# Optimization experiments

Hardware: AMD Instinct MI355X
Metric: run time of the kernel (lower is better)

The kernel has to match this reference:

```python
import jax, jax.numpy as jnp
import numpy as np

B, S, E, D, H = 4, 1024, 1024, 1024, 16   # batch, dec_seq, enc_seq, d_model, n_heads
DH = D // H
DFF = 4096
EPS = 1e-5


def setup_inputs() -> dict:
    key = jax.random.key(0)
    ks = jax.random.split(key, 16)
    w = lambda k, shp: (jax.random.normal(k, shp, dtype=jnp.float32) * 0.02)
    return {
        "x": jax.random.normal(ks[0], (B, S, D), dtype=jnp.float32),
        "enc_x": jax.random.normal(ks[1], (B, E, D), dtype=jnp.float32),
        # masked self-attn (fused qkv)
        "w_qkv": w(ks[2], (D, 3 * D)), "b_qkv": jnp.zeros((3 * D,), jnp.float32),
        "w_sa_o": w(ks[3], (D, D)), "b_sa_o": jnp.zeros((D,), jnp.float32),
        # cross-attn
        "w_q": w(ks[4], (D, D)), "b_q": jnp.zeros((D,), jnp.float32),
        "w_k": w(ks[5], (D, D)), "b_k": jnp.zeros((D,), jnp.float32),
        "w_v": w(ks[6], (D, D)), "b_v": jnp.zeros((D,), jnp.float32),
        "w_ca_o": w(ks[7], (D, D)), "b_ca_o": jnp.zeros((D,), jnp.float32),
        # ffn
        "w1": w(ks[8], (D, DFF)), "b1": jnp.zeros((DFF,), jnp.float32),
        "w2": w(ks[9], (DFF, D)), "b2": jnp.zeros((D,), jnp.float32),
        # layernorms
        "g1": jnp.ones((D,), jnp.float32), "be1": jnp.zeros((D,), jnp.float32),
        "g2": jnp.ones((D,), jnp.float32), "be2": jnp.zeros((D,), jnp.float32),
        "g3": jnp.ones((D,), jnp.float32), "be3": jnp.zeros((D,), jnp.float32),
    }


def _layernorm(x, g, b):
    mean = jnp.mean(x, axis=-1, keepdims=True)
    var = jnp.mean(jnp.square(x - mean), axis=-1, keepdims=True)  # unbiased=False
    return g * (x - mean) / jnp.sqrt(var + EPS) + b


def _masked_self_attn(x, w_qkv, b_qkv, w_o, b_o):
    b, s, d = x.shape
    qkv = x @ w_qkv + b_qkv                            # [b,s,3D]
    # Faithful to torch: view as [b,s,H,3*DH] then chunk last dim (interleaved per-head).
    qkv = qkv.reshape(b, s, H, 3 * DH).transpose(0, 2, 1, 3)   # [b,H,s,3DH]
    q, k, v = jnp.split(qkv, 3, axis=-1)               # each [b,H,s,DH]
    scores = jnp.einsum('bhqd,bhkd->bhqk', q, k) / jnp.sqrt(jnp.float32(DH))
    mask = jnp.triu(jnp.ones((s, s), dtype=bool), k=1)
    scores = jnp.where(mask, -jnp.inf, scores)
    attn = jax.nn.softmax(scores, axis=-1)
    out = jnp.einsum('bhqk,bhkd->bhqd', attn, v)       # [b,H,s,DH]
    out = out.transpose(0, 2, 1, 3).reshape(b, s, d)
    return out @ w_o + b_o


def _cross_attn(dec_x, enc_x, w_q, b_q, w_k, b_k, w_v, b_v, w_o, b_o):
    b, sq, d = dec_x.shape
    sk = enc_x.shape[1]
    q = (dec_x @ w_q + b_q).reshape(b, sq, H, DH).transpose(0, 2, 1, 3)
    k = (enc_x @ w_k + b_k).reshape(b, sk, H, DH).transpose(0, 2, 1, 3)
    v = (enc_x @ w_v + b_v).reshape(b, sk, H, DH).transpose(0, 2, 1, 3)
    scores = jnp.einsum('bhqd,bhkd->bhqk', q, k) / jnp.sqrt(jnp.float32(DH))
    attn = jax.nn.softmax(scores, axis=-1)
    out = jnp.einsum('bhqk,bhkd->bhqd', attn, v).transpose(0, 2, 1, 3).reshape(b, sq, d)
    return out @ w_o + b_o


def reference(x, enc_x, w_qkv, b_qkv, w_sa_o, b_sa_o,
              w_q, b_q, w_k, b_k, w_v, b_v, w_ca_o, b_ca_o,
              w1, b1, w2, b2, g1, be1, g2, be2, g3, be3):
    h = _layernorm(x + _masked_self_attn(x, w_qkv, b_qkv, w_sa_o, b_sa_o), g1, be1)
    h = _layernorm(h + _cross_attn(h, enc_x, w_q, b_q, w_k, b_k, w_v, b_v, w_ca_o, b_ca_o), g2, be2)
    ffn = jax.nn.gelu(h @ w1 + b1, approximate=False) @ w2 + b2  # torch F.gelu default = exact
    return _layernorm(h + ffn, g3, be3)
```

## Files before the change

### kernel.cpp

```cpp
#include <hip/hip_runtime.h>

#define BB 4
#define SS 1024
#define DD 1024
#define HH 16
#define DHH 64
#define DFF 4096
#define MROWS 4096
#define NEG_BIG (-1e30f)
#define LOG2E 1.4426950408889634f
#define SCL_L2E 0.1803368801111244f

typedef float  f32x4  __attribute__((ext_vector_type(4)));
typedef __bf16 bf16x8 __attribute__((ext_vector_type(8)));
typedef __bf16 bf16x4 __attribute__((ext_vector_type(4)));

#define DEV __device__ __forceinline__

DEV void glds16(const __bf16* g, __bf16* l) {
  __builtin_amdgcn_global_load_lds((__attribute__((address_space(1))) void*)(g),
                                   (__attribute__((address_space(3))) void*)(l),
                                   16, 0, 0);
}

DEV float sanit(float v) {
  return fminf(fmaxf(v, -1e30f), 1e30f);
}

DEV float gelu_f(float v) {
  const float z  = fabsf(v) * 0.70710678118654752f;
  const float t  = __builtin_amdgcn_rcpf(1.f + 0.3275911f * z);
  float poly = ((((1.061405429f * t - 1.453152027f) * t + 1.421413741f) * t
                 - 0.284496736f) * t + 0.254829592f) * t;
  float er = 1.f - poly * __expf(-z * z);
  er = copysignf(er, v);
  return 0.5f * v * (1.f + er);
}

__global__ __launch_bounds__(256) void cvt_bf16(const float* __restrict__ src,
                                                __bf16* __restrict__ dst)
{
  const int idx = blockIdx.x * 256 + threadIdx.x;
  const f32x4 v = ((const f32x4*)src)[idx];
  bf16x4 o;
#pragma unroll
  for (int i = 0; i < 4; i++) o[i] = (__bf16)v[i];
  ((bf16x4*)dst)[idx] = o;
}

__global__ __launch_bounds__(256) void wtrans(const float* __restrict__ src,
                                              __bf16* __restrict__ dst,
                                              int K, int N)
{
  __shared__ float t[64][65];
  const int k0 = blockIdx.y * 64, n0 = blockIdx.x * 64;
  const int c = threadIdx.x & 63, r0 = threadIdx.x >> 6;
#pragma unroll
  for (int i = 0; i < 16; i++) {
    const int r = r0 * 16 + i;
    t[r][c] = src[(size_t)(k0 + r) * N + n0 + c];
  }
  __syncthreads();
#pragma unroll
  for (int i = 0; i < 16; i++) {
    const int r = r0 * 16 + i;
    dst[(size_t)(n0 + r) * K + k0 + c] = (__bf16)t[c][r];
  }
}

__global__ __launch_bounds__(256) void vtrans(const __bf16* __restrict__ src,
                                              int stride, int colMul, int colAdd,
                                              __bf16* __restrict__ dst)
{
  __shared__ __bf16 t[64][66];
  const int bh = blockIdx.y, b = bh >> 4, h = bh & 15;
  const int s0 = blockIdx.x * 64;
  const int c = threadIdx.x & 63, r0 = threadIdx.x >> 6;
  const __bf16* sp = src + (size_t)(b * SS) * stride + h * colMul + colAdd;
#pragma unroll
  for (int i = 0; i < 16; i++) {
    const int s = r0 * 16 + i;
    t[s][c] = sp[(size_t)(s0 + s) * stride + c];
  }
  __syncthreads();
  __bf16* dp = dst + (size_t)bh * 64 * 1024;
#pragma unroll
  for (int i = 0; i < 16; i++) {
    const int d = r0 * 16 + i;
    dp[(size_t)d * 1024 + s0 + c] = t[c][d];
  }
}

template<int MODE, int SPLIT>
__global__ __launch_bounds__(512) void gemm256(
    const __bf16* __restrict__ A, const __bf16* __restrict__ Bt,
    const float* __restrict__ bias, void* __restrict__ Cout,
    int N, int K)
{
  __shared__ __align__(16) __bf16 As[2][2][2][128 * 32];
  __shared__ __align__(16) __bf16 Bs[2][2][2][128 * 32];

  const int gx = gridDim.x;
  const int nwg = gx * gridDim.y;
  int idl = blockIdx.x + gx * blockIdx.y;
  idl = (idl & 7) * (nwg >> 3) + (idl >> 3);
  const int bn = (idl % gx) * 256, bm = (idl / gx) * 256;
  const int kz = SPLIT ? blockIdx.z : 0;
  const int Keff = SPLIT ? (K >> 1) : K;
  const int kOff = SPLIT ? kz * Keff : 0;

  const int tid = threadIdx.x, wid = tid >> 6, lane = tid & 63;
  const int quad = lane >> 4, ln = lane & 15;
  const int wr = (wid >> 2) * 128, wc = (wid & 3) * 64;
  const int mh = wid >> 2;
  const int nh = (wid & 3) >> 1;
  const int rbB = wc & 64;
  const int sw = ln >> 2;

  const int srow = tid >> 2;
  const int scol = ((tid & 3) ^ ((tid >> 4) & 3)) * 8;
  const __bf16* gA = A  + (size_t)(bm + srow) * K + kOff + scol;
  const __bf16* gB = Bt + (size_t)(bn + srow) * K + kOff + scol;
  const int dOff = tid * 8;

#define STG(bf_, MATG, MATS, kh_, kt_) do {                                         \
    glds16(MATG + (size_t)(kt_) * 64 + (kh_) * 32,                 &MATS[bf_][0][kh_][0] + dOff); \
    glds16(MATG + (size_t)128 * K + (size_t)(kt_) * 64 + (kh_) * 32, &MATS[bf_][1][kh_][0] + dOff); \
  } while (0)

#define LD_A(dst, p_, i_, ks_) \
  dst = *(const bf16x8*)(&As[p_][mh][ks_][0] + ((i_) * 16 + ln) * 32 + ((quad ^ sw) * 8))
#define LD_B(dst, p_, j_, ks_) \
  dst = *(const bf16x8*)(&Bs[p_][nh][ks_][0] + (rbB + (j_) * 16 + ln) * 32 + ((quad ^ sw) * 8))

  f32x4 acc[8][4];
#pragma unroll
  for (int i = 0; i < 8; i++)
#pragma unroll
    for (int j = 0; j < 4; j++) acc[i][j] = (f32x4){0.f, 0.f, 0.f, 0.f};

  const int nkt = Keff >> 6;
  STG(0, gA, As, 0, 0); STG(0, gB, Bs, 0, 0);
  STG(0, gA, As, 1, 0); STG(0, gB, Bs, 1, 0);

  for (int tt = 0; tt < nkt; ++tt) {
    const int p = tt & 1, pn = p ^ 1;
    const int ktn = (tt + 1 < nkt) ? (tt + 1) : tt;
    bf16x8 af[4], bfr[4];

    STG(pn, gA, As, 0, ktn);
    asm volatile("s_waitcnt vmcnt(6)" ::: "memory");
    __builtin_amdgcn_sched_barrier(0);
    __builtin_amdgcn_s_barrier();
#pragma unroll
    for (int j = 0; j < 4; j++) LD_B(bfr[j], p, j, 0);
#pragma unroll
    for (int i = 0; i < 4; i++) LD_A(af[i], p, i, 0);
    asm volatile("s_waitcnt lgkmcnt(0)" ::: "memory");
    __builtin_amdgcn_sched_barrier(0);
    __builtin_amdgcn_s_setprio(1);
#pragma unroll
    for (int i = 0; i < 4; i++)
#pragma unroll
      for (int j = 0; j < 4; j++)
        acc[i][j] = __builtin_amdgcn_mfma_f32_16x16x32_bf16(af[i], bfr[j], acc[i][j], 0, 0, 0);
    __builtin_amdgcn_s_setprio(0);

    STG(pn, gB, Bs, 0, ktn);
#pragma unroll
    for (int i = 0; i < 4; i++) LD_A(af[i], p, i + 4, 0);
    asm volatile("s_waitcnt lgkmcnt(0)" ::: "memory");
    __builtin_amdgcn_sched_barrier(0);
    __builtin_amdgcn_s_setprio(1);
#pragma unroll
    for (int i = 0; i < 4; i++)
#pragma unroll
      for (int j = 0; j < 4; j++)
        acc[i + 4][j] = __builtin_amdgcn_mfma_f32_16x16x32_bf16(af[i], bfr[j], acc[i + 4][j], 0, 0, 0);
    __builtin_amdgcn_s_setprio(0);

    STG(pn, gA, As, 1, ktn);
    asm volatile("s_waitcnt vmcnt(6)" ::: "memory");
    __builtin_amdgcn_sched_barrier(0);
    __builtin_amdgcn_s_barrier();
#pragma unroll
    for (int j = 0; j < 4; j++) LD_B(bfr[j], p, j, 1);
#pragma unroll
    for (int i = 0; i < 4; i++) LD_A(af[i], p, i, 1);
    asm volatile("s_waitcnt lgkmcnt(0)" ::: "memory");
    __builtin_amdgcn_sched_barrier(0);
    __builtin_amdgcn_s_setprio(1);
#pragma unroll
    for (int i = 0; i < 4; i++)
#pragma unroll
      for (int j = 0; j < 4; j++)
        acc[i][j] = __builtin_amdgcn_mfma_f32_16x16x32_bf16(af[i], bfr[j], acc[i][j], 0, 0, 0);
    __builtin_amdgcn_s_setprio(0);

    STG(pn, gB, Bs, 1, ktn);
#pragma unroll
    for (int i = 0; i < 4; i++) LD_A(af[i], p, i + 4, 1);
    asm volatile("s_waitcnt lgkmcnt(0)" ::: "memory");
    __builtin_amdgcn_sched_barrier(0);
    __builtin_amdgcn_s_setprio(1);
#pragma unroll
    for (int i = 0; i < 4; i++)
#pragma unroll
      for (int j = 0; j < 4; j++)
        acc[i + 4][j] = __builtin_amdgcn_mfma_f32_16x16x32_bf16(af[i], bfr[j], acc[i + 4][j], 0, 0, 0);
    __builtin_amdgcn_s_setprio(0);
    __builtin_amdgcn_s_barrier();
  }
#undef STG
#undef LD_A
#undef LD_B

  float* outF = (float*)Cout + (SPLIT ? (size_t)kz * MROWS * N : 0);
#pragma unroll
  for (int j = 0; j < 4; j++) {
    const int col = bn + wc + j * 16 + ln;
    const float bv = (SPLIT && kz) ? 0.f : bias[col];
#pragma unroll
    for (int i = 0; i < 8; i++) {
#pragma unroll
      for (int r = 0; r < 4; r++) {
        const int row = bm + wr + i * 16 + quad * 4 + r;
        float v = sanit(acc[i][j][r] + bv);
        if (MODE == 1) v = gelu_f(v);
        if (MODE == 3 && (col % 192) < 64) v *= SCL_L2E;
        if (MODE == 2) outF[(size_t)row * N + col] = v;
        else           ((__bf16*)Cout)[(size_t)row * N + col] = (__bf16)v;
      }
    }
  }
}

template<int MODE>
__global__ __launch_bounds__(256) void gemm_bt(
    const __bf16* __restrict__ A, const __bf16* __restrict__ Bt,
    const float* __restrict__ bias, const float* __restrict__ bias2,
    void* __restrict__ Cout, int N, int K)
{
  __shared__ __align__(16) __bf16 As[2][128 * 32];
  __shared__ __align__(16) __bf16 Bs[2][128 * 32];

  const int bm = blockIdx.y * 128, bn = blockIdx.x * 128;
  const int tid = threadIdx.x, wid = tid >> 6, lane = tid & 63;
  const int quad = lane >> 4, ln = lane & 15;

  const __bf16* gA = A  + (size_t)(bm + wid * 32 + (lane >> 2)) * K + (lane & 3) * 8;
  const __bf16* gB = Bt + (size_t)(bn + wid * 32 + (lane >> 2)) * K + (lane & 3) * 8;
  const int soff = (wid * 32) * 32;

  f32x4 acc[4][4];
#pragma unroll
  for (int i = 0; i < 4; i++)
#pragma unroll
    for (int j = 0; j < 4; j++) acc[i][j] = (f32x4){0.f, 0.f, 0.f, 0.f};

  const int wr = (wid >> 1) * 64, wc = (wid & 1) * 64;

#define G_STAGE(buf, kt) do {                                     \
    const int k0_ = (kt) * 32;                                    \
    glds16(gA + k0_,          &As[buf][soff]);                    \
    glds16(gA + 16 * K + k0_, &As[buf][soff + 16 * 32]);          \
    glds16(gB + k0_,          &Bs[buf][soff]);                    \
    glds16(gB + 16 * K + k0_, &Bs[buf][soff + 16 * 32]);          \
  } while (0)

#define G_COMP(buf) do {                                                    \
    bf16x8 af[4], bfr[4];                                                   \
    _Pragma("unroll")                                                       \
    for (int i = 0; i < 4; i++)                                             \
      af[i] = *(const bf16x8*)(&As[buf][(wr + i * 16 + ln) * 32 + quad * 8]); \
    _Pragma("unroll")                                                       \
    for (int j = 0; j < 4; j++)                                             \
      bfr[j] = *(const bf16x8*)(&Bs[buf][(wc + j * 16 + ln) * 32 + quad * 8]); \
    _Pragma("unroll")                                                       \
    for (int i = 0; i < 4; i++)                                             \
      _Pragma("unroll")                                                     \
      for (int j = 0; j < 4; j++)                                           \
        acc[i][j] = __builtin_amdgcn_mfma_f32_16x16x32_bf16(af[i], bfr[j], acc[i][j], 0, 0, 0); \
  } while (0)

  const int nk = K >> 5;
  G_STAGE(0, 0);
  __syncthreads();
  for (int kt = 0; kt < nk; kt += 2) {
    G_STAGE(1, kt + 1);
    G_COMP(0);
    __syncthreads();
    if (kt + 2 < nk) G_STAGE(0, kt + 2);
    G_COMP(1);
    __syncthreads();
  }
#undef G_STAGE
#undef G_COMP

#pragma unroll
  for (int j = 0; j < 4; j++) {
    const int col = bn + wc + j * 16 + ln;
    float bv;
    if (MODE == 4) bv = (col < 1024) ? bias[col] : bias2[col - 1024];
    else           bv = bias[col];
#pragma unroll
    for (int i = 0; i < 4; i++) {
#pragma unroll
      for (int r = 0; r < 4; r++) {
        const int row = bm + wr + i * 16 + quad * 4 + r;
        float v = sanit(acc[i][j][r] + bv);
        if (MODE == 1) v = gelu_f(v);
        if (MODE == 3 && (col % 192) < 64) v *= SCL_L2E;
        if (MODE == 2) ((float*)Cout)[(size_t)row * N + col] = v;
        else           ((__bf16*)Cout)[(size_t)row * N + col] = (__bf16)v;
      }
    }
  }
}

template<int MODE>
__global__ __launch_bounds__(256) void gemm_bt64(
    const __bf16* __restrict__ A, const __bf16* __restrict__ Bt,
    const float* __restrict__ bias, void* __restrict__ Cout,
    int N, int K)
{
  __shared__ __align__(16) __bf16 As[2][128 * 32];
  __shared__ __align__(16) __bf16 Bs[2][64 * 32];

  const int bm = blockIdx.y * 128, bn = blockIdx.x * 64;
  const int tid = threadIdx.x, wid = tid >> 6, lane = tid & 63;
  const int quad = lane >> 4, ln = lane & 15;

  const __bf16* gA = A  + (size_t)(bm + wid * 32 + (lane >> 2)) * K + (lane & 3) * 8;
  const __bf16* gB = Bt + (size_t)(bn + wid * 16 + (lane >> 2)) * K + (lane & 3) * 8;
  const int aoff = (wid * 32) * 32;
  const int boff = (wid * 16) * 32;

  f32x4 acc[4][2];
#pragma unroll
  for (int i = 0; i < 4; i++)
#pragma unroll
    for (int j = 0; j < 2; j++) acc[i][j] = (f32x4){0.f, 0.f, 0.f, 0.f};

  const int wr = (wid >> 1) * 64, wc = (wid & 1) * 32;

#define G_STAGE(buf, kt) do {                                     \
    const int k0_ = (kt) * 32;                                    \
    glds16(gA + k0_,          &As[buf][aoff]);                    \
    glds16(gA + 16 * K + k0_, &As[buf][aoff + 16 * 32]);          \
    glds16(gB + k0_,          &Bs[buf][boff]);                    \
  } while (0)

#define G_COMP(buf) do {                                                    \
    bf16x8 af[4], bfr[2];                                                   \
    _Pragma("unroll")                                                       \
    for (int i = 0; i < 4; i++)                                             \
      af[i] = *(const bf16x8*)(&As[buf][(wr + i * 16 + ln) * 32 + quad * 8]); \
    _Pragma("unroll")                                                       \
    for (int j = 0; j < 2; j++)                                             \
      bfr[j] = *(const bf16x8*)(&Bs[buf][(wc + j * 16 + ln) * 32 + quad * 8]); \
    _Pragma("unroll")                                                       \
    for (int i = 0; i < 4; i++)                                             \
      _Pragma("unroll")                                                     \
      for (int j = 0; j < 2; j++)                                           \
        acc[i][j] = __builtin_amdgcn_mfma_f32_16x16x32_bf16(af[i], bfr[j], acc[i][j], 0, 0, 0); \
  } while (0)

  const int nk = K >> 5;
  G_STAGE(0, 0);
  __syncthreads();
  for (int kt = 0; kt < nk; kt += 2) {
    G_STAGE(1, kt + 1);
    G_COMP(0);
    __syncthreads();
    if (kt + 2 < nk) G_STAGE(0, kt + 2);
    G_COMP(1);
    __syncthreads();
  }
#undef G_STAGE
#undef G_COMP

#pragma unroll
  for (int j = 0; j < 2; j++) {
    const int col = bn + wc + j * 16 + ln;
    const float bv = bias[col];
#pragma unroll
    for (int i = 0; i < 4; i++) {
#pragma unroll
      for (int r = 0; r < 4; r++) {
        const int row = bm + wr + i * 16 + quad * 4 + r;
        float v = sanit(acc[i][j][r] + bv);
        if (MODE == 3) v *= SCL_L2E;
        if (MODE == 2) ((float*)Cout)[(size_t)row * N + col] = v;
        else           ((__bf16*)Cout)[(size_t)row * N + col] = (__bf16)v;
      }
    }
  }
}

__global__ __launch_bounds__(256) void attn(
    const __bf16* __restrict__ qp, int qStride, int qMul, int qAdd,
    const __bf16* __restrict__ kp, int kStride, int kMul, int kAdd,
    const __bf16* __restrict__ vt, __bf16* __restrict__ outp, int causal)
{
  __shared__ __align__(16) __bf16 Kt[2][64 * 64];
  __shared__ __align__(16) __bf16 Vt[2][64 * 64];
  __shared__ __align__(16) __bf16 ptl[4][32 * 64];

  const int id = blockIdx.x;
  const int bh = ((id >> 6) << 3) | (id & 7);
  const int qblk = (id >> 3) & 7;
  const int b = bh >> 4, h = bh & 15;
  const int tid = threadIdx.x, wid = tid >> 6, lane = tid & 63;
  const int quad = lane >> 4, ln = lane & 15;
  const int qbase = qblk * 128;
  const int rowb0 = qbase + wid * 32;
  const int rowTop = rowb0 + 31;

  bf16x8 aq[2][2];
#pragma unroll
  for (int rf = 0; rf < 2; ++rf) {
    const __bf16* qr = qp + (size_t)(b * SS + rowb0 + rf * 16 + ln) * qStride
                          + h * qMul + qAdd;
#pragma unroll
    for (int ks = 0; ks < 2; ++ks)
      aq[rf][ks] = *(const bf16x8*)(qr + ks * 32 + quad * 8);
  }

  f32x4 acc[2][4];
#pragma unroll
  for (int rf = 0; rf < 2; ++rf)
#pragma unroll
    for (int nb = 0; nb < 4; ++nb) acc[rf][nb] = (f32x4){0.f, 0.f, 0.f, 0.f};
  float l_r[2][4] = {{0.f,0.f,0.f,0.f},{0.f,0.f,0.f,0.f}};

  const __bf16* kbase = kp + (size_t)(b * SS) * kStride + h * kMul + kAdd;
  const __bf16* vtb = vt + (size_t)bh * 64 * 1024;
  __bf16* ptw = ptl[wid];

  const int kvEnd = causal ? (qbase + 128) : SS;
  const int nT = kvEnd >> 6;

  const int sr = wid * 16 + (lane >> 3);
  const int sq = lane & 7;

#pragma unroll
  for (int p = 0; p < 2; ++p) {
    const int r = sr + p * 8;
    const int qs = (sq ^ (r & 7)) * 8;
    glds16(kbase + (size_t)r * kStride + qs, Kt[0] + (wid * 2 + p) * 512);
    glds16(vtb + (size_t)r * 1024 + qs,      Vt[0] + (wid * 2 + p) * 512);
  }

  for (int t = 0; t < nT; ++t) {
    const int cur = t & 1;
    const int kv0 = t * 64;

    if (t + 1 < nT) {
      const int kn = kv0 + 64;
#pragma unroll
      for (int p = 0; p < 2; ++p) {
        const int r = sr + p * 8;
        const int qs = (sq ^ (r & 7)) * 8;
        glds16(kbase + (size_t)(kn + r) * kStride + qs, Kt[cur ^ 1] + (wid * 2 + p) * 512);
        glds16(vtb + (size_t)r * 1024 + kn + qs,        Vt[cur ^ 1] + (wid * 2 + p) * 512);
      }
      __asm__ volatile("s_waitcnt vmcnt(4)" ::: "memory");
    } else {
      __asm__ volatile("s_waitcnt vmcnt(0)" ::: "memory");
    }
    __builtin_amdgcn_sched_barrier(0);
    __builtin_amdgcn_s_barrier();
    __asm__ volatile("" ::: "memory");
    __builtin_amdgcn_sched_barrier(0);

    if (!causal || kv0 <= rowTop) {
      const __bf16* kt = Kt[cur];
      const __bf16* vv = Vt[cur];

      f32x4 sc[2][4];
      {
        bf16x8 kf[4][2];
#pragma unroll
        for (int c = 0; c < 4; ++c) {
          const int row = c * 16 + ln;
#pragma unroll
          for (int ks = 0; ks < 2; ++ks)
            kf[c][ks] = *(const bf16x8*)(kt + row * 64 + (((ks * 4 + quad) ^ (ln & 7)) * 8));
        }
#pragma unroll
        for (int rf = 0; rf < 2; ++rf)
#pragma unroll
          for (int c = 0; c < 4; ++c) {
            f32x4 s_ = (f32x4){0.f, 0.f, 0.f, 0.f};
            s_ = __builtin_amdgcn_mfma_f32_16x16x32_bf16(aq[rf][0], kf[c][0], s_, 0, 0, 0);
            s_ = __builtin_amdgcn_mfma_f32_16x16x32_bf16(aq[rf][1], kf[c][1], s_, 0, 0, 0);
            sc[rf][c] = s_;
          }
      }

#pragma unroll
      for (int rf = 0; rf < 2; ++rf) {
        const bool doMask = causal && (kv0 + 63 > rowb0 + rf * 16);
#pragma unroll
        for (int r = 0; r < 4; ++r) {
          const int rowg = rowb0 + rf * 16 + quad * 4 + r;
          float p[4];
#pragma unroll
          for (int c = 0; c < 4; ++c) {
            float e = sc[rf][c][r];
            if (doMask && (kv0 + c * 16 + ln > rowg)) e = NEG_BIG;
            p[c] = exp2f(e);
          }
          l_r[rf][r] += (p[0] + p[1]) + (p[2] + p[3]);
          const int m = rf * 16 + quad * 4 + r;
          __bf16* pr = ptw + m * 64;
#pragma unroll
          for (int c = 0; c < 4; ++c) {
            const int col = c * 16 + ln;
            pr[(((col >> 3) ^ (m & 7)) << 3) + (col & 7)] = (__bf16)p[c];
          }
        }
      }
      __asm__ volatile("s_waitcnt lgkmcnt(0)" ::: "memory");
      __builtin_amdgcn_sched_barrier(0);

      {
        bf16x8 pa[2][2];
#pragma unroll
        for (int rf = 0; rf < 2; ++rf) {
          const int m = rf * 16 + ln;
#pragma unroll
          for (int ks = 0; ks < 2; ++ks)
            pa[rf][ks] = *(const bf16x8*)(ptw + m * 64 + (((ks * 4 + quad) ^ (m & 7)) * 8));
        }
#pragma unroll
        for (int nb = 0; nb < 4; ++nb) {
          const int vrow = nb * 16 + ln;
          const bf16x8 vf0 = *(const bf16x8*)(vv + vrow * 64 + (((quad)     ^ (ln & 7)) * 8));
          const bf16x8 vf1 = *(const bf16x8*)(vv + vrow * 64 + (((4 + quad) ^ (ln & 7)) * 8));
#pragma unroll
          for (int rf = 0; rf < 2; ++rf) {
            acc[rf][nb] = __builtin_amdgcn_mfma_f32_16x16x32_bf16(pa[rf][0], vf0, acc[rf][nb], 0, 0, 0);
            acc[rf][nb] = __builtin_amdgcn_mfma_f32_16x16x32_bf16(pa[rf][1], vf1, acc[rf][nb], 0, 0, 0);
          }
        }
      }
    }

    __asm__ volatile("" ::: "memory");
    __builtin_amdgcn_sched_barrier(0);
    __builtin_amdgcn_s_barrier();
  }

#pragma unroll
  for (int rf = 0; rf < 2; ++rf) {
#pragma unroll
    for (int r = 0; r < 4; ++r) {
      float l = l_r[rf][r];
#pragma unroll
      for (int off = 1; off < 16; off <<= 1) l += __shfl_xor(l, off, 64);
      const float inv = 1.f / fmaxf(l, 1e-30f);
      const int rowg = rowb0 + rf * 16 + quad * 4 + r;
      __bf16* op = outp + (size_t)(b * SS + rowg) * DD + h * 64;
#pragma unroll
      for (int nb = 0; nb < 4; ++nb)
        op[nb * 16 + ln] = (__bf16)sanit(acc[rf][nb][r] * inv);
    }
  }
}

__global__ __launch_bounds__(256) void ln_k(
    const float* __restrict__ residf, const float* __restrict__ proj,
    const float* __restrict__ proj2,
    const float* __restrict__ g, const float* __restrict__ be,
    float* __restrict__ outf, __bf16* __restrict__ outb)
{
  const int row = blockIdx.x, tid = threadIdx.x;
  const f32x4 pb = ((const f32x4*)(proj   + (size_t)row * 1024))[tid];
  const f32x4 rb = ((const f32x4*)(residf + (size_t)row * 1024))[tid];
  f32x4 x;
#pragma unroll
  for (int i = 0; i < 4; i++) x[i] = pb[i] + rb[i];
  if (proj2) {
    const f32x4 qb_ = ((const f32x4*)(proj2 + (size_t)row * 1024))[tid];
#pragma unroll
    for (int i = 0; i < 4; i++) x[i] += qb_[i];
  }
#pragma unroll
  for (int i = 0; i < 4; i++)
    x[i] = fminf(fmaxf(x[i], -1e15f), 1e15f);
  float s  = x[0] + x[1] + x[2] + x[3];
  float ss = x[0]*x[0] + x[1]*x[1] + x[2]*x[2] + x[3]*x[3];
#pragma unroll
  for (int off = 1; off < 64; off <<= 1) {
    s  += __shfl_xor(s,  off, 64);
    ss += __shfl_xor(ss, off, 64);
  }
  __shared__ float sm[8];
  if ((tid & 63) == 0) { sm[tid >> 6] = s; sm[4 + (tid >> 6)] = ss; }
  __syncthreads();
  s  = sm[0] + sm[1] + sm[2] + sm[3];
  ss = sm[4] + sm[5] + sm[6] + sm[7];
  const float mean = s * (1.f / 1024.f);
  const float var  = fmaxf(ss * (1.f / 1024.f) - mean * mean, 0.f);
  const float rstd = rsqrtf(var + 1e-5f);
  const int c = tid * 4;
  f32x4 o;
#pragma unroll
  for (int i = 0; i < 4; i++)
    o[i] = g[c + i] * ((x[i] - mean) * rstd) + be[c + i];
  if (outf) ((f32x4*)(outf + (size_t)row * 1024))[tid] = o;
  if (outb) {
    bf16x4 ob;
#pragma unroll
    for (int i = 0; i < 4; i++) ob[i] = (__bf16)o[i];
    ((bf16x4*)(outb + (size_t)row * 1024))[tid] = ob;
  }
}

extern "C" void kernel_launch(void* const* d_in, const int* in_sizes, int n_in,
                              void* d_out, int out_size, void* d_ws, size_t ws_size,
                              hipStream_t stream)
{
  const float* x      = (const float*)d_in[0];
  const float* enc    = (const float*)d_in[1];
  const float* w_qkv  = (const float*)d_in[2];
  const float* b_qkv  = (const float*)d_in[3];
  const float* w_sa_o = (const float*)d_in[4];
  const float* b_sa_o = (const float*)d_in[5];
  const float* w_q    = (const float*)d_in[6];
  const float* b_q    = (const float*)d_in[7];
  const float* w_k    = (const float*)d_in[8];
  const float* b_k    = (const float*)d_in[9];
  const float* w_v    = (const float*)d_in[10];
  const float* b_v    = (const float*)d_in[11];
  const float* w_ca_o = (const float*)d_in[12];
  const float* b_ca_o = (const float*)d_in[13];
  const float* w1     = (const float*)d_in[14];
  const float* b1     = (const float*)d_in[15];
  const float* w2     = (const float*)d_in[16];
  const float* b2     = (const float*)d_in[17];
  const float* g1     = (const float*)d_in[18];
  const float* be1    = (const float*)d_in[19];
  const float* g2     = (const float*)d_in[20];
  const float* be2    = (const float*)d_in[21];
  const float* g3     = (const float*)d_in[22];
  const float* be3    = (const float*)d_in[23];

  const size_t MB = 1024 * 1024;
  char* base = (char*)d_ws;
  __bf16* wqkvT = (__bf16*)(base + 0 * MB);
  __bf16* wsaoT = (__bf16*)(base + 6 * MB);
  __bf16* wqT   = (__bf16*)(base + 8 * MB);
  __bf16* wkvT  = (__bf16*)(base + 10 * MB);
  __bf16* wkT   = (__bf16*)(base + 10 * MB);
  __bf16* wvT   = (__bf16*)(base + 12 * MB);
  __bf16* wcaoT = (__bf16*)(base + 14 * MB);
  __bf16* w1T   = (__bf16*)(base + 0 * MB);
  __bf16* w2T   = (__bf16*)(base + 8 * MB);
  __bf16* xb    = (__bf16*)(base + 16 * MB);
  __bf16* encb  = (__bf16*)(base + 24 * MB);
  __bf16* qkv   = (__bf16*)(base + 32 * MB);
  __bf16* kvb   = (__bf16*)(base + 32 * MB);
  __bf16* qcab  = (__bf16*)(base + 48 * MB);
  __bf16* vt    = (__bf16*)(base + 56 * MB);
  __bf16* mid   = (__bf16*)(base + 32 * MB);
  __bf16* attnb = (__bf16*)(base + 64 * MB);
  float*  proj  = (float*) (base + 72 * MB);
  float*  h1f   = (float*) (base + 88 * MB);
  __bf16* h1b   = (__bf16*)(base + 104 * MB);
  float*  h2f   = (float*) (base + 112 * MB);
  __bf16* h2b   = (__bf16*)(base + 128 * MB);
  (void)wkT; (void)wvT;

  cvt_bf16<<<4096, 256, 0, stream>>>(x,   xb);
  cvt_bf16<<<4096, 256, 0, stream>>>(enc, encb);
  wtrans<<<dim3(48, 16), 256, 0, stream>>>(w_qkv,  wqkvT, 1024, 3072);
  wtrans<<<dim3(16, 16), 256, 0, stream>>>(w_sa_o, wsaoT, 1024, 1024);
  wtrans<<<dim3(16, 16), 256, 0, stream>>>(w_q,    wqT,   1024, 1024);
  wtrans<<<dim3(16, 16), 256, 0, stream>>>(w_k,    wkT,   1024, 1024);
  wtrans<<<dim3(16, 16), 256, 0, stream>>>(w_v,    wvT,   1024, 1024);
  wtrans<<<dim3(16, 16), 256, 0, stream>>>(w_ca_o, wcaoT, 1024, 1024);

  gemm256<3,0><<<dim3(12, 16), 512, 0, stream>>>(xb, wqkvT, b_qkv, qkv, 3072, 1024);
  vtrans<<<dim3(16, 64), 256, 0, stream>>>(qkv, 3072, 192, 128, vt);
  attn<<<512, 256, 0, stream>>>(qkv, 3072, 192, 0,
                                qkv, 3072, 192, 64, vt, attnb, 1);
  gemm_bt64<2><<<dim3(16, 32), 256, 0, stream>>>(attnb, wsaoT, b_sa_o, proj, 1024, 1024);
  ln_k<<<4096, 256, 0, stream>>>(x, proj, nullptr, g1, be1, h1f, h1b);

  gemm_bt64<3><<<dim3(16, 32), 256, 0, stream>>>(h1b, wqT, b_q, qcab, 1024, 1024);
  gemm_bt<4><<<dim3(16, 32), 256, 0, stream>>>(encb, wkvT, b_k, b_v, kvb, 2048, 1024);
  vtrans<<<dim3(16, 64), 256, 0, stream>>>(kvb, 2048, 64, 1024, vt);
  attn<<<512, 256, 0, stream>>>(qcab, 1024, 64, 0,
                                kvb, 2048, 64, 0, vt, attnb, 0);
  gemm_bt64<2><<<dim3(16, 32), 256, 0, stream>>>(attnb, wcaoT, b_ca_o, proj, 1024, 1024);
  ln_k<<<4096, 256, 0, stream>>>(h1f, proj, nullptr, g2, be2, h2f, h2b);

  wtrans<<<dim3(64, 16), 256, 0, stream>>>(w1, w1T, 1024, 4096);
  wtrans<<<dim3(16, 64), 256, 0, stream>>>(w2, w2T, 4096, 1024);
  gemm256<1,0><<<dim3(16, 16), 512, 0, stream>>>(h2b, w1T, b1, mid, 4096, 1024);
  gemm256<2,1><<<dim3(4, 16, 2), 512, 0, stream>>>(mid, w2T, b2, proj, 1024, 4096);
  ln_k<<<4096, 256, 0, stream>>>(h2f, proj, proj + (size_t)MROWS * 1024,
                                 g3, be3, (float*)d_out, nullptr);

  (void)in_sizes; (void)n_in; (void)out_size; (void)ws_size;
}
```

Baseline: 576.1 us.

## Restructure GEMM main loop: issue all prefetches upfront, single barrier per k-tile

The GEMM main loop is rewritten so that all four global-to-LDS prefetch stages for the next k-tile are issued together at the top, followed by one wait and one barrier. The previous four-phase interleaving of staging, LDS reads and MFMA blocks is replaced by a simple loop over the two k-substeps, with the compiler left to schedule the LDS reads and MFMAs. The intent is fewer barriers and waits per tile and better overlap of loads with compute. It drops the explicit s_setprio hints and the manual interleaving, and it relies on the vmcnt(8) count being correct for the current tile's data to have landed.

```diff
diff --git a/kernel.cpp b/kernel.cpp
--- a/kernel.cpp
+++ b/kernel.cpp
@@ -146,70 +146,35 @@
   for (int tt = 0; tt < nkt; ++tt) {
     const int p = tt & 1, pn = p ^ 1;
     const int ktn = (tt + 1 < nkt) ? (tt + 1) : tt;
-    bf16x8 af[4], bfr[4];
-
-    STG(pn, gA, As, 0, ktn);
-    asm volatile("s_waitcnt vmcnt(6)" ::: "memory");
+
+    STG(pn, gA, As, 0, ktn); STG(pn, gB, Bs, 0, ktn);
+    STG(pn, gA, As, 1, ktn); STG(pn, gB, Bs, 1, ktn);
+    __builtin_amdgcn_sched_barrier(0);
+    asm volatile("s_waitcnt vmcnt(8)" ::: "memory");
     __builtin_amdgcn_sched_barrier(0);
     __builtin_amdgcn_s_barrier();
-#pragma unroll
-    for (int j = 0; j < 4; j++) LD_B(bfr[j], p, j, 0);
-#pragma unroll
-    for (int i = 0; i < 4; i++) LD_A(af[i], p, i, 0);
-    asm volatile("s_waitcnt lgkmcnt(0)" ::: "memory");
-    __builtin_amdgcn_sched_barrier(0);
-    __builtin_amdgcn_s_setprio(1);
-#pragma unroll
-    for (int i = 0; i < 4; i++)
-#pragma unroll
-      for (int j = 0; j < 4; j++)
-        acc[i][j] = __builtin_amdgcn_mfma_f32_16x16x32_bf16(af[i], bfr[j], acc[i][j], 0, 0, 0);
-    __builtin_amdgcn_s_setprio(0);
-
-    STG(pn, gB, Bs, 0, ktn);
-#pragma unroll
-    for (int i = 0; i < 4; i++) LD_A(af[i], p, i + 4, 0);
-    asm volatile("s_waitcnt lgkmcnt(0)" ::: "memory");
-    __builtin_amdgcn_sched_barrier(0);
-    __builtin_amdgcn_s_setprio(1);
-#pragma unroll
-    for (int i = 0; i < 4; i++)
-#pragma unroll
-      for (int j = 0; j < 4; j++)
-        acc[i + 4][j] = __builtin_amdgcn_mfma_f32_16x16x32_bf16(af[i], bfr[j], acc[i + 4][j], 0, 0, 0);
-    __builtin_amdgcn_s_setprio(0);
-
-    STG(pn, gA, As, 1, ktn);
-    asm volatile("s_waitcnt vmcnt(6)" ::: "memory");
-    __builtin_amdgcn_sched_barrier(0);
+    asm volatile("" ::: "memory");
+    __builtin_amdgcn_sched_barrier(0);
+
+#pragma unroll
+    for (int ks = 0; ks < 2; ++ks) {
+      bf16x8 bfr[4];
+#pragma unroll
+      for (int j = 0; j < 4; j++) LD_B(bfr[j], p, j, ks);
+#pragma unroll
+      for (int i = 0; i < 8; i++) {
+        bf16x8 a;
+        LD_A(a, p, i, ks);
+#pragma unroll
+        for (int j = 0; j < 4; j++)
+          acc[i][j] = __builtin_amdgcn_mfma_f32_16x16x32_bf16(a, bfr[j], acc[i][j], 0, 0, 0);
+      }
+    }
+
+    __builtin_amdgcn_sched_barrier(0);
+    asm volatile("" ::: "memory");
     __builtin_amdgcn_s_barrier();
-#pragma unroll
-    for (int j = 0; j < 4; j++) LD_B(bfr[j], p, j, 1);
-#pragma unroll
-    for (int i = 0; i < 4; i++) LD_A(af[i], p, i, 1);
-    asm volatile("s_waitcnt lgkmcnt(0)" ::: "memory");
-    __builtin_amdgcn_sched_barrier(0);
-    __builtin_amdgcn_s_setprio(1);
-#pragma unroll
-    for (int i = 0; i < 4; i++)
-#pragma unroll
-      for (int j = 0; j < 4; j++)
-        acc[i][j] = __builtin_amdgcn_mfma_f32_16x16x32_bf16(af[i], bfr[j], acc[i][j], 0, 0, 0);
-    __builtin_amdgcn_s_setprio(0);
-
-    STG(pn, gB, Bs, 1, ktn);
-#pragma unroll
-    for (int i = 0; i < 4; i++) LD_A(af[i], p, i + 4, 1);
-    asm volatile("s_waitcnt lgkmcnt(0)" ::: "memory");
-    __builtin_amdgcn_sched_barrier(0);
-    __builtin_amdgcn_s_setprio(1);
-#pragma unroll
-    for (int i = 0; i < 4; i++)
-#pragma unroll
-      for (int j = 0; j < 4; j++)
-        acc[i + 4][j] = __builtin_amdgcn_mfma_f32_16x16x32_bf16(af[i], bfr[j], acc[i + 4][j], 0, 0, 0);
-    __builtin_amdgcn_s_setprio(0);
-    __builtin_amdgcn_s_barrier();
+    __builtin_amdgcn_sched_barrier(0);
   }
 #undef STG
 #undef LD_A
```

Result: no change. 583.1 us (+1.2%).
